# Performance work log

Hardware: AMD Instinct MI355X
Metric: run time of the kernel (lower is better)

The kernel has to match this reference:

```python
import jax, jax.numpy as jnp
import numpy as np

B, U, L, H, M = 4, 16, 128, 768, 256   # docs, utterances/doc, tokens/utt, hidden, mentions/doc
HID = 150                               # Score MLP hidden dim
N_CLUSTERS = 32


def setup_inputs() -> dict:
    key = jax.random.key(0)
    ks = jax.random.split(key, 8)
    hidden = jax.random.normal(ks[0], (B, U, L, H), jnp.float32)

    rng = np.random.default_rng(0)
    span_utt = rng.integers(0, U, (B, M))
    span_start = rng.integers(0, L - 8, (B, M))
    span_end = span_start + rng.integers(1, 9, (B, M))  # span length in [1, 8]

    # coreference labels: label[i, j] = 1 iff j is a true antecedent (j < i, same cluster);
    # if mention i has no antecedent, label[i, i] = 1 (the epsilon / new-entity slot).
    clusters = rng.integers(0, N_CLUSTERS, (B, M))
    same = clusters[:, :, None] == clusters[:, None, :]
    ant = same & np.tril(np.ones((M, M), bool), -1)
    labels = ant.astype(np.float32)
    diag = np.arange(M)
    labels[:, diag, diag] = (~ant.any(-1)).astype(np.float32)

    scale = 0.02
    W1 = jax.random.normal(ks[1], (3 * H, HID), jnp.float32) * scale
    W2 = jax.random.normal(ks[2], (HID, HID), jnp.float32) * scale
    W3 = jax.random.normal(ks[3], (HID, 1), jnp.float32) * scale
    return {
        "hidden": hidden,
        "span_utt": jnp.asarray(span_utt, jnp.int32),
        "span_start": jnp.asarray(span_start, jnp.int32),
        "span_end": jnp.asarray(span_end, jnp.int32),
        "labels": jnp.asarray(labels),
        "W1": W1, "b1": jnp.zeros((HID,), jnp.float32),
        "W2": W2, "b2": jnp.zeros((HID,), jnp.float32),
        "W3": W3, "b3": jnp.zeros((1,), jnp.float32),
    }


def reference(hidden, span_utt, span_start, span_end, labels, W1, b1, W2, b2, W3, b3):
    # ---- span mean-pooling (EntityEncoder, aggr='mean') ----
    pos = jnp.arange(L)
    mask = (pos[None, None, :] >= span_start[..., None]) & (pos[None, None, :] < span_end[..., None])
    w = mask.astype(hidden.dtype) / (span_end - span_start)[..., None].astype(hidden.dtype)  # [B,M,L]
    gathered = jnp.take_along_axis(hidden, span_utt[:, :, None, None], axis=1)  # [B,M,L,H]
    pooled = jnp.einsum('bml,bmlh->bmh', w, gathered)  # [B,M,H]

    # ---- pairwise antecedent scoring (PairScorer / Score MLP, dropout=eval) ----
    ii, jj = np.tril_indices(M, -1)  # static pair indices, P = M(M-1)/2
    # concat(i_g, j_g, i_g*j_g) @ W1  ==  i_g@W1a + j_g@W1b + (i_g*j_g)@W1c
    W1a, W1b, W1c = W1[:H], W1[H:2 * H], W1[2 * H:]
    hi = pooled @ W1a   # [B,M,HID]
    hj = pooled @ W1b   # [B,M,HID]
    prod = pooled[:, ii] * pooled[:, jj]                    # [B,P,H]
    h1 = jax.nn.relu(hi[:, ii] + hj[:, jj] + prod @ W1c + b1)
    h2 = jax.nn.relu(h1 @ W2 + b2)
    s = (h2 @ W3 + b3)[..., 0]  # [B,P]

    # ---- per-mention ragged softmax, padded to [M, M] with -1000 ----
    # row i has logits s_ij for j<i plus epsilon=0 at j=i (diagonal of zeros matrix)
    logits = jnp.zeros((B, M, M), hidden.dtype).at[:, ii, jj].set(s)
    valid = jnp.tril(jnp.ones((M, M), bool))
    probs = jax.nn.softmax(jnp.where(valid, logits, -1e30), axis=-1)
    probs = jnp.where(valid, probs, jnp.asarray(-1000.0, hidden.dtype))

    # ---- compute_loss ----
    eps = 1e-8
    prob_sum = jnp.sum(jnp.clip(probs * labels, eps, 1.0 - eps), axis=-1)  # [B,M]
    loss = -jnp.sum(jnp.log(prob_sum))
    return loss
```

## Files before the change

### kernel.cpp

```cpp
#include <hip/hip_runtime.h>
#include <hip/hip_bf16.h>

#define B_ 4
#define U_ 16
#define L_ 128
#define H_ 768
#define M_ 256
#define HID_ 150

typedef _Float16 half8 __attribute__((ext_vector_type(8)));
typedef _Float16 half4t __attribute__((ext_vector_type(4)));
typedef float floatx4 __attribute__((ext_vector_type(4)));
typedef float floatx16 __attribute__((ext_vector_type(16)));

__device__ __forceinline__ void gl_lds16(const _Float16* g, _Float16* l)
{
    __builtin_amdgcn_global_load_lds(
        (const __attribute__((address_space(1))) unsigned int*)g,
        (__attribute__((address_space(3))) unsigned int*)l, 16, 0, 0);
}

__global__ __launch_bounds__(256) void prep_kernel(
    const float* __restrict__ W1, const float* __restrict__ W2,
    const float* __restrict__ b2, const float* __restrict__ W3,
    _Float16* __restrict__ W1cs, _Float16* __restrict__ W2s,
    _Float16* __restrict__ W1abs, float2* __restrict__ bw)
{
    int idx = blockIdx.x * 256 + threadIdx.x;
    if (blockIdx.x == 0 && threadIdx.x < 160) {
        int n = threadIdx.x;
        bw[n] = (n < HID_) ? make_float2(b2[n], W3[n]) : make_float2(0.f, 0.f);
    }
    if (idx < 122880) {
        int k = idx / 160, n = idx - k * 160;
        float v = (n < HID_) ? W1[(size_t)(2 * H_ + k) * HID_ + n] : 0.f;
        W1cs[(k >> 4) * 2560 + (n >> 5) * 512 +
             (((n & 31) | (((k >> 3) & 1) << 5)) << 3) + (k & 7)] = (_Float16)v;
        return;
    }
    idx -= 122880;
    if (idx < 25600) {
        int k = idx / 160, n = idx - k * 160;
        float v = (k < HID_ && n < HID_) ? W2[(size_t)k * HID_ + n] : 0.f;
        W2s[(k >> 4) * 2560 + (n >> 5) * 512 +
            (((n & 31) | (((k >> 3) & 1) << 5)) << 3) + (k & 7)] = (_Float16)v;
        return;
    }
    idx -= 25600;
    if (idx < 245760) {
        int k = idx / 320, n = idx - k * 320;
        float v = 0.f;
        if (n < HID_) v = W1[(size_t)k * HID_ + n];
        else if (n >= 160 && n < 160 + HID_) v = W1[(size_t)(H_ + k) * HID_ + (n - 160)];
        W1abs[(k >> 5) * 10240 + (n >> 4) * 512 +
              (((n & 15) | (((k >> 3) & 3) << 4)) << 3) + (k & 7)] = (_Float16)v;
    }
}

__global__ __launch_bounds__(256) void pool_kernel(
    const float* __restrict__ hidden, const int* __restrict__ sutt,
    const int* __restrict__ sstart, const int* __restrict__ send,
    _Float16* __restrict__ pooledh)
{
    const int bm = blockIdx.x * 4 + (threadIdx.x >> 6);
    const int lane = threadIdx.x & 63;
    const int b  = bm >> 8;
    const int u  = sutt[bm];
    const int st = sstart[bm];
    const int en = send[bm];
    const float inv = 1.0f / (float)(en - st);
    const float* src = hidden + ((size_t)(b * U_ + u) * L_) * H_ + lane * 12;
    float4 s[3];
    #pragma unroll
    for (int q = 0; q < 3; ++q) s[q] = make_float4(0.f, 0.f, 0.f, 0.f);
    for (int l = st; l < en; ++l) {
        const float* p = src + (size_t)l * H_;
        #pragma unroll
        for (int q = 0; q < 3; ++q) {
            float4 v = *(const float4*)(p + q * 4);
            s[q].x += v.x; s[q].y += v.y; s[q].z += v.z; s[q].w += v.w;
        }
    }
    _Float16* gp = pooledh + (size_t)bm * H_ + lane * 12;
    #pragma unroll
    for (int q = 0; q < 3; ++q) {
        half4t hv;
        hv[0] = (_Float16)(s[q].x * inv); hv[1] = (_Float16)(s[q].y * inv);
        hv[2] = (_Float16)(s[q].z * inv); hv[3] = (_Float16)(s[q].w * inv);
        *(half4t*)(gp + q * 4) = hv;
    }
}

__global__ __launch_bounds__(256) void hihj_kernel(
    const _Float16* __restrict__ pooledh, const float* __restrict__ b1,
    const _Float16* __restrict__ W1abs,
    float* __restrict__ hiF, float* __restrict__ hjT)
{
    __shared__ __align__(16) _Float16 spool[16 * 776];
    const int blk = blockIdx.x;
    const int tid = threadIdx.x;
    for (int e = tid; e < 16 * 96; e += 256) {
        int r = e / 96, c = e - r * 96;
        *(half8*)&spool[r * 776 + c * 8] =
            *(const half8*)&pooledh[(size_t)(blk * 16 + r) * H_ + c * 8];
    }
    __syncthreads();

    const int w = tid >> 6, lane = tid & 63;
    const int g = lane >> 4, l15 = lane & 15;
    floatx4 acc[5];
    #pragma unroll
    for (int u5 = 0; u5 < 5; ++u5) acc[u5] = (floatx4){0.f, 0.f, 0.f, 0.f};
    const _Float16* aB = &spool[l15 * 776 + g * 8];
    for (int kc = 0; kc < 24; ++kc) {
        half8 av = *(const half8*)(aB + kc * 32);
        #pragma unroll
        for (int u5 = 0; u5 < 5; ++u5) {
            const int u = w * 5 + u5;
            half8 bv = *(const half8*)(W1abs + (size_t)((kc * 20 + u) * 64 + lane) * 8);
            acc[u5] = __builtin_amdgcn_mfma_f32_16x16x32_f16(av, bv, acc[u5], 0, 0, 0);
        }
    }
    const int row0 = blk * 16 + g * 4;
    #pragma unroll
    for (int u5 = 0; u5 < 5; ++u5) {
        const int n = (w * 5 + u5) * 16 + l15;
        if (n < HID_) {
            float b1v = b1[n];
            #pragma unroll
            for (int r = 0; r < 4; ++r)
                hiF[(size_t)(row0 + r) * 160 + n] = acc[u5][r] + b1v;
        } else if (n >= 160 && n < 160 + HID_) {
            *(float4*)&hjT[(size_t)(n - 160) * 1024 + row0] =
                make_float4(acc[u5][0], acc[u5][1], acc[u5][2], acc[u5][3]);
        }
    }
}

__global__ __launch_bounds__(128, 2) void pair_mlp_kernel(
    const _Float16* __restrict__ pooledh,
    const float* __restrict__ hiF, const float* __restrict__ hjT,
    const _Float16* __restrict__ W1cs, const _Float16* __restrict__ W2s,
    const float2* __restrict__ bw, const float* __restrict__ b3,
    float* __restrict__ logits)
{
    __shared__ __align__(16) _Float16 smem[2 * 5440];

    int q = blockIdx.x;
    const int b = q / 576;
    int r = q - b * 576;
    int jt = 0;
    while (r >= 128 - 16 * jt) { r -= 128 - 16 * jt; ++jt; }
    const int p = 16 * jt + r;
    const int i0 = 2 * p, j0 = jt * 32;
    const int bm = b * M_;
    const int w = threadIdx.x >> 6;
    const int lane = threadIdx.x & 63;
    const int c31 = lane & 31;
    const int hw = lane >> 5;

    _Float16* Wb0 = smem;
    _Float16* Wb1 = smem + 5120;
    _Float16* h1w = smem + w * 5440;

    const _Float16* pjp = pooledh + (size_t)(bm + j0 + c31) * H_ + (hw << 3);
    const _Float16* pip = pooledh + (size_t)(bm + i0 + w) * H_ + (hw << 3);

    floatx16 acc1[5];
    #pragma unroll
    for (int t1 = 0; t1 < 5; ++t1)
        #pragma unroll
        for (int e = 0; e < 16; ++e) acc1[t1][e] = 0.f;

    {
        const _Float16* gW = W1cs + (size_t)(5 * w) * 512 + lane * 8;
        #pragma unroll
        for (int c = 0; c < 5; ++c)
            gl_lds16(gW + c * 512, Wb0 + (5 * w + c) * 512);
    }
    half8 Apj0 = *(const half8*)(pjp);
    half8 Apj1 = *(const half8*)(pjp + 16);
    half8 Ai0  = *(const half8*)(pip);
    half8 Ai1  = *(const half8*)(pip + 16);
    __syncthreads();

    for (int kc = 0; kc < 24; ++kc) {
        const _Float16* Wcur = (kc & 1) ? Wb1 : Wb0;
        _Float16*       Wnxt = (kc & 1) ? Wb0 : Wb1;
        half8 npj0, npj1, ni0, ni1;
        if (kc < 23) {
            const _Float16* gW = W1cs + (size_t)(kc + 1) * 5120 + (5 * w) * 512 + lane * 8;
            #pragma unroll
            for (int c = 0; c < 5; ++c)
                gl_lds16(gW + c * 512, Wnxt + (5 * w + c) * 512);
            const int kb = (kc + 1) * 32;
            npj0 = *(const half8*)(pjp + kb);
            npj1 = *(const half8*)(pjp + kb + 16);
            ni0  = *(const half8*)(pip + kb);
            ni1  = *(const half8*)(pip + kb + 16);
        }
        {
            half8 a = Ai0 * Apj0;
            #pragma unroll
            for (int t1 = 0; t1 < 5; ++t1) {
                half8 wf = *(const half8*)&Wcur[t1 * 512 + lane * 8];
                acc1[t1] = __builtin_amdgcn_mfma_f32_32x32x16_f16(wf, a, acc1[t1], 0, 0, 0);
            }
        }
        {
            half8 a = Ai1 * Apj1;
            #pragma unroll
            for (int t1 = 0; t1 < 5; ++t1) {
                half8 wf = *(const half8*)&Wcur[(5 + t1) * 512 + lane * 8];
                acc1[t1] = __builtin_amdgcn_mfma_f32_32x32x16_f16(wf, a, acc1[t1], 0, 0, 0);
            }
        }
        if (kc < 23) { Apj0 = npj0; Apj1 = npj1; Ai0 = ni0; Ai1 = ni1; }
        __syncthreads();
    }

    const int jcol = bm + j0 + c31;
    #pragma unroll
    for (int t1 = 0; t1 < 5; ++t1) {
        #pragma unroll
        for (int qd = 0; qd < 4; ++qd) {
            const int n1 = t1 * 32 + 8 * qd + 4 * hw;
            float hj0 = hjT[(size_t)(n1 + 0) * 1024 + jcol];
            float hj1 = hjT[(size_t)(n1 + 1) * 1024 + jcol];
            float hj2 = hjT[(size_t)(n1 + 2) * 1024 + jcol];
            float hj3 = hjT[(size_t)(n1 + 3) * 1024 + jcol];
            float4 hiv = *(const float4*)&hiF[(size_t)(bm + i0 + w) * 160 + n1];
            half4t hv;
            hv[0] = (_Float16)fmaxf(acc1[t1][4 * qd + 0] + hiv.x + hj0, 0.f);
            hv[1] = (_Float16)fmaxf(acc1[t1][4 * qd + 1] + hiv.y + hj1, 0.f);
            hv[2] = (_Float16)fmaxf(acc1[t1][4 * qd + 2] + hiv.z + hj2, 0.f);
            hv[3] = (_Float16)fmaxf(acc1[t1][4 * qd + 3] + hiv.w + hj3, 0.f);
            *(half4t*)&h1w[c31 * 170 + n1] = hv;
        }
    }
    __syncthreads();

    const float b3v = b3[0];
    floatx16 acc2[5];
    #pragma unroll
    for (int t2 = 0; t2 < 5; ++t2)
        #pragma unroll
        for (int e = 0; e < 16; ++e) acc2[t2][e] = 0.f;

    half8 W2b[2][5], h1b[2];
    #pragma unroll
    for (int c = 0; c < 2; ++c) {
        const _Float16* wb = W2s + (size_t)(c * 5) * 512 + lane * 8;
        #pragma unroll
        for (int t2 = 0; t2 < 5; ++t2) W2b[c][t2] = *(const half8*)(wb + t2 * 512);
        h1b[c] = *(const half8*)&h1w[c31 * 170 + c * 16 + hw * 8];
    }
    for (int kc2 = 0; kc2 < 10; ++kc2) {
        const int cur = kc2 & 1;
        half8 nw[5], nh;
        if (kc2 < 8) {
            const _Float16* wb = W2s + (size_t)((kc2 + 2) * 5) * 512 + lane * 8;
            #pragma unroll
            for (int t2 = 0; t2 < 5; ++t2) nw[t2] = *(const half8*)(wb + t2 * 512);
            nh = *(const half8*)&h1w[c31 * 170 + (kc2 + 2) * 16 + hw * 8];
        }
        #pragma unroll
        for (int t2 = 0; t2 < 5; ++t2)
            acc2[t2] = __builtin_amdgcn_mfma_f32_32x32x16_f16(
                W2b[cur][t2], h1b[cur], acc2[t2], 0, 0, 0);
        if (kc2 < 8) {
            #pragma unroll
            for (int t2 = 0; t2 < 5; ++t2) W2b[cur][t2] = nw[t2];
            h1b[cur] = nh;
        }
    }

    float sown = 0.f;
    #pragma unroll
    for (int t2 = 0; t2 < 5; ++t2) {
        #pragma unroll
        for (int qd = 0; qd < 4; ++qd) {
            const int n2 = t2 * 32 + 8 * qd + 4 * hw;
            float4 bw01 = *(const float4*)&bw[n2];
            float4 bw23 = *(const float4*)&bw[n2 + 2];
            sown += fmaxf(acc2[t2][4 * qd + 0] + bw01.x, 0.f) * bw01.y;
            sown += fmaxf(acc2[t2][4 * qd + 1] + bw01.z, 0.f) * bw01.w;
            sown += fmaxf(acc2[t2][4 * qd + 2] + bw23.x, 0.f) * bw23.y;
            sown += fmaxf(acc2[t2][4 * qd + 3] + bw23.z, 0.f) * bw23.w;
        }
    }
    float s = sown + __shfl_xor(sown, 32);
    const int i = i0 + w;
    const int j = j0 + c31;
    if (lane < 32 && j < i)
        logits[(size_t)(bm + i) * M_ + j] = s + b3v;
}

__global__ __launch_bounds__(256) void loss_kernel(
    const float* __restrict__ logits, const float* __restrict__ labels,
    float* __restrict__ out)
{
    const int bm = blockIdx.x;
    const int i  = bm & (M_ - 1);
    const int j  = threadIdx.x;
    __shared__ float red[4];
    __shared__ float bcast;

    float val = (j < i) ? logits[(size_t)bm * M_ + j]
                        : ((j == i) ? 0.0f : -1e30f);

    float m = val;
    #pragma unroll
    for (int off = 32; off >= 1; off >>= 1) m = fmaxf(m, __shfl_down(m, off, 64));
    const int wave = j >> 6, lane = j & 63;
    if (lane == 0) red[wave] = m;
    __syncthreads();
    if (j == 0) bcast = fmaxf(fmaxf(red[0], red[1]), fmaxf(red[2], red[3]));
    __syncthreads();
    const float mm = bcast;

    float e = (j <= i) ? expf(val - mm) : 0.0f;
    float s = e;
    #pragma unroll
    for (int off = 32; off >= 1; off >>= 1) s += __shfl_down(s, off, 64);
    __syncthreads();
    if (lane == 0) red[wave] = s;
    __syncthreads();
    if (j == 0) bcast = red[0] + red[1] + red[2] + red[3];
    __syncthreads();
    const float ssum = bcast;

    float prob = (j <= i) ? (e / ssum) : -1000.0f;
    float lab = labels[(size_t)bm * M_ + j];
    float tv = prob * lab;
    tv = fminf(fmaxf(tv, 1e-8f), 1.0f - 1e-8f);
    float rs = tv;
    #pragma unroll
    for (int off = 32; off >= 1; off >>= 1) rs += __shfl_down(rs, off, 64);
    __syncthreads();
    if (lane == 0) red[wave] = rs;
    __syncthreads();
    if (j == 0) atomicAdd(out, -logf(red[0] + red[1] + red[2] + red[3]));
}

extern "C" void kernel_launch(void* const* d_in, const int* in_sizes, int n_in,
                              void* d_out, int out_size, void* d_ws, size_t ws_size,
                              hipStream_t stream)
{
    const float* hidden = (const float*)d_in[0];
    const int*   sutt   = (const int*)d_in[1];
    const int*   sstart = (const int*)d_in[2];
    const int*   send   = (const int*)d_in[3];
    const float* labels = (const float*)d_in[4];
    const float* W1     = (const float*)d_in[5];
    const float* b1     = (const float*)d_in[6];
    const float* W2     = (const float*)d_in[7];
    const float* b2     = (const float*)d_in[8];
    const float* W3     = (const float*)d_in[9];
    const float* b3     = (const float*)d_in[10];

    float* ws = (float*)d_ws;
    float*    hiF     = ws;
    float*    hjT     = ws + 163840;
    float*    logits  = ws + 327680;
    float2*   bw      = (float2*)(ws + 589824);
    _Float16* pooledh = (_Float16*)(ws + 590144);
    _Float16* W1cs    = (_Float16*)(ws + 983360);
    _Float16* W2s     = (_Float16*)(ws + 1106240);
    _Float16* W1abs   = (_Float16*)(ws + 1119040);
    float* out = (float*)d_out;

    hipMemsetAsync(d_out, 0, sizeof(float), stream);

    prep_kernel<<<dim3(1540), 256, 0, stream>>>(W1, W2, b2, W3,
                                                W1cs, W2s, W1abs, bw);
    pool_kernel<<<dim3(256), 256, 0, stream>>>(hidden, sutt, sstart, send, pooledh);
    hihj_kernel<<<dim3(64), 256, 0, stream>>>(pooledh, b1, W1abs, hiF, hjT);
    pair_mlp_kernel<<<dim3(576 * B_), 128, 0, stream>>>(pooledh, hiF, hjT,
                                                        W1cs, W2s, bw, b3, logits);
    loss_kernel<<<dim3(B_ * M_), 256, 0, stream>>>(logits, labels, out);
}
```

Before: 202.2 us.

## Merge prep and pool kernels, split hihj blocks, single-wave loss, raise occupancy

Folds the span-pooling work into the weight-prep kernel as extra blocks, removing one launch and letting the two independent jobs run concurrently. The hihj kernel is split into 256 one-wave blocks, each covering a quarter of the output columns, to spread work over more CUs at the cost of reloading the pooled rows four times. The loss kernel becomes a single wave per row that handles four elements per lane with xor shuffles, removing shared-memory reductions and barriers. pair_mlp's launch bound is raised to three blocks per SIMD, which may force register spilling.

```diff
diff --git a/kernel.cpp b/kernel.cpp
--- a/kernel.cpp
+++ b/kernel.cpp
@@ -20,12 +20,45 @@
         (__attribute__((address_space(3))) unsigned int*)l, 16, 0, 0);
 }
 
-__global__ __launch_bounds__(256) void prep_kernel(
+__global__ __launch_bounds__(256) void prep_pool_kernel(
     const float* __restrict__ W1, const float* __restrict__ W2,
     const float* __restrict__ b2, const float* __restrict__ W3,
+    const float* __restrict__ hidden, const int* __restrict__ sutt,
+    const int* __restrict__ sstart, const int* __restrict__ send,
     _Float16* __restrict__ W1cs, _Float16* __restrict__ W2s,
-    _Float16* __restrict__ W1abs, float2* __restrict__ bw)
-{
+    _Float16* __restrict__ W1abs, float2* __restrict__ bw,
+    _Float16* __restrict__ pooledh)
+{
+    if (blockIdx.x >= 1540) {
+        const int bm = (blockIdx.x - 1540) * 4 + (threadIdx.x >> 6);
+        const int lane = threadIdx.x & 63;
+        const int b  = bm >> 8;
+        const int u  = sutt[bm];
+        const int st = sstart[bm];
+        const int en = send[bm];
+        const float inv = 1.0f / (float)(en - st);
+        const float* src = hidden + ((size_t)(b * U_ + u) * L_) * H_ + lane * 12;
+        float4 s[3];
+        #pragma unroll
+        for (int q = 0; q < 3; ++q) s[q] = make_float4(0.f, 0.f, 0.f, 0.f);
+        for (int l = st; l < en; ++l) {
+            const float* p = src + (size_t)l * H_;
+            #pragma unroll
+            for (int q = 0; q < 3; ++q) {
+                float4 v = *(const float4*)(p + q * 4);
+                s[q].x += v.x; s[q].y += v.y; s[q].z += v.z; s[q].w += v.w;
+            }
+        }
+        _Float16* gp = pooledh + (size_t)bm * H_ + lane * 12;
+        #pragma unroll
+        for (int q = 0; q < 3; ++q) {
+            half4t hv;
+            hv[0] = (_Float16)(s[q].x * inv); hv[1] = (_Float16)(s[q].y * inv);
+            hv[2] = (_Float16)(s[q].z * inv); hv[3] = (_Float16)(s[q].w * inv);
+            *(half4t*)(gp + q * 4) = hv;
+        }
+        return;
+    }
     int idx = blockIdx.x * 256 + threadIdx.x;
     if (blockIdx.x == 0 && threadIdx.x < 160) {
         int n = threadIdx.x;
@@ -57,56 +90,23 @@
     }
 }
 
-__global__ __launch_bounds__(256) void pool_kernel(
-    const float* __restrict__ hidden, const int* __restrict__ sutt,
-    const int* __restrict__ sstart, const int* __restrict__ send,
-    _Float16* __restrict__ pooledh)
-{
-    const int bm = blockIdx.x * 4 + (threadIdx.x >> 6);
-    const int lane = threadIdx.x & 63;
-    const int b  = bm >> 8;
-    const int u  = sutt[bm];
-    const int st = sstart[bm];
-    const int en = send[bm];
-    const float inv = 1.0f / (float)(en - st);
-    const float* src = hidden + ((size_t)(b * U_ + u) * L_) * H_ + lane * 12;
-    float4 s[3];
-    #pragma unroll
-    for (int q = 0; q < 3; ++q) s[q] = make_float4(0.f, 0.f, 0.f, 0.f);
-    for (int l = st; l < en; ++l) {
-        const float* p = src + (size_t)l * H_;
-        #pragma unroll
-        for (int q = 0; q < 3; ++q) {
-            float4 v = *(const float4*)(p + q * 4);
-            s[q].x += v.x; s[q].y += v.y; s[q].z += v.z; s[q].w += v.w;
-        }
-    }
-    _Float16* gp = pooledh + (size_t)bm * H_ + lane * 12;
-    #pragma unroll
-    for (int q = 0; q < 3; ++q) {
-        half4t hv;
-        hv[0] = (_Float16)(s[q].x * inv); hv[1] = (_Float16)(s[q].y * inv);
-        hv[2] = (_Float16)(s[q].z * inv); hv[3] = (_Float16)(s[q].w * inv);
-        *(half4t*)(gp + q * 4) = hv;
-    }
-}
-
-__global__ __launch_bounds__(256) void hihj_kernel(
+__global__ __launch_bounds__(64) void hihj_kernel(
     const _Float16* __restrict__ pooledh, const float* __restrict__ b1,
     const _Float16* __restrict__ W1abs,
     float* __restrict__ hiF, float* __restrict__ hjT)
 {
     __shared__ __align__(16) _Float16 spool[16 * 776];
-    const int blk = blockIdx.x;
+    const int rowgrp = blockIdx.x >> 2;
+    const int nq     = blockIdx.x & 3;
     const int tid = threadIdx.x;
-    for (int e = tid; e < 16 * 96; e += 256) {
+    for (int e = tid; e < 16 * 96; e += 64) {
         int r = e / 96, c = e - r * 96;
         *(half8*)&spool[r * 776 + c * 8] =
-            *(const half8*)&pooledh[(size_t)(blk * 16 + r) * H_ + c * 8];
+            *(const half8*)&pooledh[(size_t)(rowgrp * 16 + r) * H_ + c * 8];
     }
     __syncthreads();
 
-    const int w = tid >> 6, lane = tid & 63;
+    const int lane = tid;
     const int g = lane >> 4, l15 = lane & 15;
     floatx4 acc[5];
     #pragma unroll
@@ -116,15 +116,15 @@
         half8 av = *(const half8*)(aB + kc * 32);
         #pragma unroll
         for (int u5 = 0; u5 < 5; ++u5) {
-            const int u = w * 5 + u5;
+            const int u = nq * 5 + u5;
             half8 bv = *(const half8*)(W1abs + (size_t)((kc * 20 + u) * 64 + lane) * 8);
             acc[u5] = __builtin_amdgcn_mfma_f32_16x16x32_f16(av, bv, acc[u5], 0, 0, 0);
         }
     }
-    const int row0 = blk * 16 + g * 4;
+    const int row0 = rowgrp * 16 + g * 4;
     #pragma unroll
     for (int u5 = 0; u5 < 5; ++u5) {
-        const int n = (w * 5 + u5) * 16 + l15;
+        const int n = (nq * 5 + u5) * 16 + l15;
         if (n < HID_) {
             float b1v = b1[n];
             #pragma unroll
@@ -137,7 +137,7 @@
     }
 }
 
-__global__ __launch_bounds__(128, 2) void pair_mlp_kernel(
+__global__ __launch_bounds__(128, 3) void pair_mlp_kernel(
     const _Float16* __restrict__ pooledh,
     const float* __restrict__ hiF, const float* __restrict__ hjT,
     const _Float16* __restrict__ W1cs, const _Float16* __restrict__ W2s,
@@ -296,51 +296,49 @@
         logits[(size_t)(bm + i) * M_ + j] = s + b3v;
 }
 
-__global__ __launch_bounds__(256) void loss_kernel(
+__global__ __launch_bounds__(64) void loss_kernel(
     const float* __restrict__ logits, const float* __restrict__ labels,
     float* __restrict__ out)
 {
     const int bm = blockIdx.x;
     const int i  = bm & (M_ - 1);
-    const int j  = threadIdx.x;
-    __shared__ float red[4];
-    __shared__ float bcast;
-
-    float val = (j < i) ? logits[(size_t)bm * M_ + j]
-                        : ((j == i) ? 0.0f : -1e30f);
-
-    float m = val;
-    #pragma unroll
-    for (int off = 32; off >= 1; off >>= 1) m = fmaxf(m, __shfl_down(m, off, 64));
-    const int wave = j >> 6, lane = j & 63;
-    if (lane == 0) red[wave] = m;
-    __syncthreads();
-    if (j == 0) bcast = fmaxf(fmaxf(red[0], red[1]), fmaxf(red[2], red[3]));
-    __syncthreads();
-    const float mm = bcast;
-
-    float e = (j <= i) ? expf(val - mm) : 0.0f;
-    float s = e;
-    #pragma unroll
-    for (int off = 32; off >= 1; off >>= 1) s += __shfl_down(s, off, 64);
-    __syncthreads();
-    if (lane == 0) red[wave] = s;
-    __syncthreads();
-    if (j == 0) bcast = red[0] + red[1] + red[2] + red[3];
-    __syncthreads();
-    const float ssum = bcast;
-
-    float prob = (j <= i) ? (e / ssum) : -1000.0f;
-    float lab = labels[(size_t)bm * M_ + j];
-    float tv = prob * lab;
-    tv = fminf(fmaxf(tv, 1e-8f), 1.0f - 1e-8f);
-    float rs = tv;
-    #pragma unroll
-    for (int off = 32; off >= 1; off >>= 1) rs += __shfl_down(rs, off, 64);
-    __syncthreads();
-    if (lane == 0) red[wave] = rs;
-    __syncthreads();
-    if (j == 0) atomicAdd(out, -logf(red[0] + red[1] + red[2] + red[3]));
+    const int lane = threadIdx.x;
+
+    float val[4];
+    #pragma unroll
+    for (int qq = 0; qq < 4; ++qq) {
+        const int j = qq * 64 + lane;
+        val[qq] = (j < i) ? logits[(size_t)bm * M_ + j]
+                          : ((j == i) ? 0.0f : -1e30f);
+    }
+    float m = fmaxf(fmaxf(val[0], val[1]), fmaxf(val[2], val[3]));
+    #pragma unroll
+    for (int off = 32; off >= 1; off >>= 1) m = fmaxf(m, __shfl_xor(m, off));
+
+    float s = 0.f;
+    float e[4];
+    #pragma unroll
+    for (int qq = 0; qq < 4; ++qq) {
+        const int j = qq * 64 + lane;
+        e[qq] = (j <= i) ? expf(val[qq] - m) : 0.0f;
+        s += e[qq];
+    }
+    #pragma unroll
+    for (int off = 32; off >= 1; off >>= 1) s += __shfl_xor(s, off);
+    const float inv_s = 1.0f / s;
+
+    float rs = 0.f;
+    #pragma unroll
+    for (int qq = 0; qq < 4; ++qq) {
+        const int j = qq * 64 + lane;
+        float prob = (j <= i) ? (e[qq] * inv_s) : -1000.0f;
+        float tv = prob * labels[(size_t)bm * M_ + j];
+        rs += fminf(fmaxf(tv, 1e-8f), 1.0f - 1e-8f);
+    }
+    #pragma unroll
+    for (int off = 32; off >= 1; off >>= 1) rs += __shfl_xor(rs, off);
+
+    if (lane == 0) atomicAdd(out, -logf(rs));
 }
 
 extern "C" void kernel_launch(void* const* d_in, const int* in_sizes, int n_in,
@@ -372,11 +370,11 @@
 
     hipMemsetAsync(d_out, 0, sizeof(float), stream);
 
-    prep_kernel<<<dim3(1540), 256, 0, stream>>>(W1, W2, b2, W3,
-                                                W1cs, W2s, W1abs, bw);
-    pool_kernel<<<dim3(256), 256, 0, stream>>>(hidden, sutt, sstart, send, pooledh);
-    hihj_kernel<<<dim3(64), 256, 0, stream>>>(pooledh, b1, W1abs, hiF, hjT);
+    prep_pool_kernel<<<dim3(1796), 256, 0, stream>>>(
+        W1, W2, b2, W3, hidden, sutt, sstart, send,
+        W1cs, W2s, W1abs, bw, pooledh);
+    hihj_kernel<<<dim3(256), 64, 0, stream>>>(pooledh, b1, W1abs, hiF, hjT);
     pair_mlp_kernel<<<dim3(576 * B_), 128, 0, stream>>>(pooledh, hiF, hjT,
                                                         W1cs, W2s, bw, b3, logits);
-    loss_kernel<<<dim3(B_ * M_), 256, 0, stream>>>(logits, labels, out);
-}
+    loss_kernel<<<dim3(B_ * M_), 64, 0, stream>>>(logits, labels, out);
+}
```

New measurement: 205.7 us. Within noise of the previous version (+1.8%).
